# Kernel optimization log

Hardware: AMD Instinct MI355X
Metric: run time of the kernel (lower is better)

The kernel has to match this reference:

```python
import jax, jax.numpy as jnp
import numpy as np

B, S, D, H = 8, 1024, 1024, 16
DH = D // H
LN_EPS = 1e-5
SLOPE = 0.01  # nn.LeakyReLU default negative_slope


def _ln(x, g, b):
    m = x.mean(-1, keepdims=True)
    v = ((x - m) ** 2).mean(-1, keepdims=True)
    return (x - m) / jnp.sqrt(v + LN_EPS) * g + b


def _leaky(x):
    return jnp.where(x >= 0, x, SLOPE * x)


def setup_inputs() -> dict:
    key = jax.random.key(0)
    ks = jax.random.split(key, 6)
    q = jax.random.normal(ks[0], (B, S, D), dtype=jnp.float32)
    masks = jnp.ones((B, S), dtype=jnp.int32)  # all-valid mask (masked_fill is a no-op)
    w1 = jax.random.normal(ks[1], (D, D), dtype=jnp.float32) * 0.02
    b1 = jnp.zeros((D,), jnp.float32)
    w2 = jax.random.normal(ks[2], (D, D), dtype=jnp.float32) * 0.02
    b2 = jnp.zeros((D,), jnp.float32)
    ones = jnp.ones((D,), jnp.float32)
    zeros = jnp.zeros((D,), jnp.float32)
    return dict(q=q, masks=masks,
                w1=w1, b1=b1, ln1_g=ones, ln1_b=zeros,
                w2=w2, b2=b2, ln2_g=ones, ln2_b=zeros,
                anf_g=ones, anf_b=zeros,
                an1_g=ones, an1_b=zeros,
                an2_g=ones, an2_b=zeros)


def reference(q, masks, w1, b1, ln1_g, ln1_b, w2, b2, ln2_g, ln2_b,
              anf_g, anf_b, an1_g, an1_b, an2_g, an2_b):
    # --- multi-head cosine-similarity attention (k = v = q, no projections) ---
    qh = q.reshape(B, S, H, DH).transpose(0, 2, 1, 3)  # (B,H,S,DH) == separate_heads
    qn = qh / jnp.clip(jnp.linalg.norm(qh, axis=-1, keepdims=True), 1e-8)
    # cosine similarity scores, softmax over keys
    w = jax.nn.softmax(jnp.einsum('bhqd,bhkd->bhqk', qn, qn), axis=-1)
    # masked_fill AFTER softmax (faithful to source: mask per (batch, query))
    w = jnp.where(masks[:, None, :, None] == 0, jnp.float32(-1e9), w)
    heads = jnp.einsum('bhqk,bhkd->bhqd', w, qh)
    attn = heads.transpose(0, 2, 1, 3).reshape(B, S, D)  # concat_heads
    # --- add_norm1 (dropout=0.5 but eval mode => identity) ---
    y1 = _ln(q + attn, an1_g, an1_b)
    # --- PositionWiseFFN: Linear->LN->LeakyReLU x2, then internal AddNorm ---
    h = _leaky(_ln(y1 @ w1 + b1, ln1_g, ln1_b))
    y = _leaky(_ln(h @ w2 + b2, ln2_g, ln2_b))
    y2 = _ln(y1 + y, anf_g, anf_b)
    # --- add_norm2 ---
    return _ln(y1 + y2, an2_g, an2_b)
```

## Files before the change

kernel.cpp:

```cpp
#include <hip/hip_runtime.h>
#include <hip/hip_bf16.h>

#define BB 8
#define SS 1024
#define DD 1024
#define HH 16

typedef __attribute__((ext_vector_type(8))) short short8;
typedef __attribute__((ext_vector_type(8))) __bf16 bf16x8;
typedef __attribute__((ext_vector_type(4))) float f32x4;

__device__ inline float bf2f(unsigned short h){
  unsigned u = ((unsigned)h) << 16;
  return __builtin_bit_cast(float, u);
}
__device__ inline unsigned short f2bf(float f){
  unsigned u = __builtin_bit_cast(unsigned, f);
  u += 0x7fffu + ((u >> 16) & 1u);
  return (unsigned short)(u >> 16);
}
__device__ inline f32x4 mfma16(short8 a, short8 b, f32x4 c){
  return __builtin_amdgcn_mfma_f32_16x16x32_bf16(
      __builtin_bit_cast(bf16x8, a), __builtin_bit_cast(bf16x8, b), c, 0, 0, 0);
}

__global__ __launch_bounds__(256) void prep_w(const float* __restrict__ w1,
                                              const float* __restrict__ w2,
                                              unsigned short* __restrict__ w1T,
                                              unsigned short* __restrict__ w2T){
  __shared__ float tile[64][65];
  const float* src = blockIdx.z ? w2 : w1;
  unsigned short* dst = blockIdx.z ? w2T : w1T;
  int k0 = blockIdx.x * 64, n0 = blockIdx.y * 64;
  int tx = threadIdx.x & 63, ty = threadIdx.x >> 6;
#pragma unroll
  for (int r = 0; r < 16; ++r)
    tile[ty + 4*r][tx] = src[(k0 + ty + 4*r) * DD + n0 + tx];
  __syncthreads();
#pragma unroll
  for (int r = 0; r < 16; ++r)
    dst[(n0 + ty + 4*r) * DD + k0 + tx] = f2bf(tile[tx][ty + 4*r]);
}

__global__ __launch_bounds__(256) void prep_q(const float* __restrict__ q,
                                              unsigned short* __restrict__ kf,
                                              unsigned short* __restrict__ vf){
  __shared__ float tile[64][65];
  __shared__ float rinv[64];
  int bh = blockIdx.x >> 4, st = blockIdx.x & 15;
  int b = bh >> 4, h = bh & 15;
  int t = threadIdx.x;
  int tx = t & 63, ty = t >> 6;
  int srow = b * SS + st * 64;
#pragma unroll
  for (int r = 0; r < 16; ++r)
    tile[ty + 4*r][tx] = q[(size_t)(srow + ty + 4*r) * DD + h * 64 + tx];
  __syncthreads();
  {
    int s = t >> 2, p = t & 3;
    float ssum = 0.f;
#pragma unroll
    for (int i = 0; i < 16; ++i){ float v = tile[s][p*16 + i]; ssum += v * v; }
    ssum += __shfl_xor(ssum, 1);
    ssum += __shfl_xor(ssum, 2);
    if (p == 0) rinv[s] = 1.0f / fmaxf(sqrtf(ssum), 1e-8f);
  }
  __syncthreads();
#pragma unroll
  for (int v = 0; v < 2; ++v){
    int idx = t * 2 + v;
    int c_l = idx >> 6, lane = idx & 63;
    int hf = c_l & 1, ch = c_l >> 1;
    int s = ch * 16 + (lane & 15);
    int d0 = hf * 32 + (lane >> 4) * 8;
    float rv = rinv[s];
    short8 o;
#pragma unroll
    for (int e = 0; e < 8; ++e) o[e] = (short)f2bf(tile[s][d0 + e] * rv);
    *(short8*)(kf + ((size_t)(bh * 128 + st * 8 + c_l) * 64 + lane) * 8) = o;
  }
#pragma unroll
  for (int v = 0; v < 2; ++v){
    int idx = t * 2 + v;
    int kt2 = idx >> 8, db = (idx >> 6) & 3, lane = idx & 63;
    int d = db * 16 + (lane & 15);
    int k0 = kt2 * 32 + (lane >> 4) * 8;
    short8 o;
#pragma unroll
    for (int e = 0; e < 8; ++e) o[e] = (short)f2bf(tile[k0 + e][d]);
    *(short8*)(vf + ((size_t)((bh * 32 + st * 2 + kt2) * 4 + db) * 512 + lane * 8)) = o;
  }
}

__global__ __launch_bounds__(512, 8) void attn_kern(const unsigned short* __restrict__ kf,
                                                    const unsigned short* __restrict__ vf,
                                                    const int* __restrict__ masks,
                                                    unsigned short* __restrict__ attnb){
  __shared__ unsigned short Kb[2][4][64 * 8];
  __shared__ unsigned short Vb[2][4][64 * 8];
  __shared__ unsigned short Pw[8][16 * 40];
  __shared__ int anym;
  const int bh = blockIdx.x, b = bh >> 4, h = bh & 15;
  const int sq = blockIdx.y * 128;
  const int t = threadIdx.x, w = t >> 6, l = t & 63;
  const int lr = l & 15, lg = l >> 4;
  if (t == 0) anym = 0;
  __syncthreads();
  if (t < 128 && masks[b * SS + sq + t] == 0) anym = 1;

  short8 aQ[2];
#pragma unroll
  for (int hf = 0; hf < 2; ++hf)
    aQ[hf] = *(const short8*)(kf +
        ((size_t)(bh * 128 + (blockIdx.y * 8 + w) * 2 + hf) * 64 + l) * 8);

  if (w < 4){
    const unsigned short* srcK = kf + ((size_t)(bh * 128 + w) * 64 + l) * 8;
    __builtin_amdgcn_global_load_lds((const __attribute__((address_space(1))) void*)srcK,
        (__attribute__((address_space(3))) void*)(&Kb[0][w][0]), 16, 0, 0);
  } else {
    const unsigned short* srcV = vf + ((size_t)((bh * 32 + 0) * 4 + (w - 4)) * 512 + l * 8);
    __builtin_amdgcn_global_load_lds((const __attribute__((address_space(1))) void*)srcV,
        (__attribute__((address_space(3))) void*)(&Vb[0][w - 4][0]), 16, 0, 0);
  }
  __syncthreads();

  f32x4 o[4] = {};
  f32x4 rsum = {0.f, 0.f, 0.f, 0.f};
  unsigned short* pw = &Pw[w][0];

  for (int it = 0; it < 32; ++it){
    const int cur = it & 1, nxt = cur ^ 1;
    if (it + 1 < 32){
      if (w < 4){
        const unsigned short* srcK = kf + ((size_t)(bh * 128 + (it + 1) * 4 + w) * 64 + l) * 8;
        __builtin_amdgcn_global_load_lds((const __attribute__((address_space(1))) void*)srcK,
            (__attribute__((address_space(3))) void*)(&Kb[nxt][w][0]), 16, 0, 0);
      } else {
        const unsigned short* srcV = vf + ((size_t)((bh * 32 + (it + 1)) * 4 + (w - 4)) * 512 + l * 8);
        __builtin_amdgcn_global_load_lds((const __attribute__((address_space(1))) void*)srcV,
            (__attribute__((address_space(3))) void*)(&Vb[nxt][w - 4][0]), 16, 0, 0);
      }
    }
    short8 bK[2][2];
#pragma unroll
    for (int cc = 0; cc < 2; ++cc)
#pragma unroll
      for (int hf = 0; hf < 2; ++hf)
        bK[cc][hf] = *(const short8*)&Kb[cur][cc * 2 + hf][l * 8];
    f32x4 sc[2];
#pragma unroll
    for (int cc = 0; cc < 2; ++cc){
      f32x4 z = {0.f, 0.f, 0.f, 0.f};
      z = mfma16(aQ[0], bK[cc][0], z);
      z = mfma16(aQ[1], bK[cc][1], z);
      sc[cc] = z;
    }
#pragma unroll
    for (int cc = 0; cc < 2; ++cc)
#pragma unroll
      for (int j = 0; j < 4; ++j){
        float pv = __expf(sc[cc][j] - 1.0f);
        rsum[j] += pv;
        pw[(lg * 4 + j) * 40 + cc * 16 + lr] = f2bf(pv);
      }
    short8 aP = *(const short8*)&pw[lr * 40 + lg * 8];
#pragma unroll
    for (int db = 0; db < 4; ++db){
      short8 bV = *(const short8*)&Vb[cur][db][l * 8];
      o[db] = mfma16(aP, bV, o[db]);
    }
    __syncthreads();
  }

  f32x4 inv;
#pragma unroll
  for (int j = 0; j < 4; ++j){
    float r = rsum[j];
    r += __shfl_xor(r, 1); r += __shfl_xor(r, 2);
    r += __shfl_xor(r, 4); r += __shfl_xor(r, 8);
    inv[j] = 1.0f / r;
  }
#pragma unroll
  for (int db = 0; db < 4; ++db)
#pragma unroll
    for (int j = 0; j < 4; ++j){
      int row = sq + w * 16 + lg * 4 + j;
      float val = o[db][j] * inv[j];
      if (anym && masks[b * SS + row] == 0){
        float vs = 0.f;
        for (int kt = 0; kt < 32; ++kt)
          for (int part = 0; part < 4; ++part){
            const unsigned short* vp = vf +
                ((size_t)((bh * 32 + kt) * 4 + db) * 512 + (part * 16 + lr) * 8);
            for (int e = 0; e < 8; ++e) vs += bf2f(vp[e]);
          }
        val = -1e9f * vs;
      }
      attnb[(size_t)(b * SS + row) * DD + h * 64 + db * 16 + lr] = f2bf(val);
    }
}

__device__ inline float2 block_reduce2(float a, float bq){
  __shared__ float sm[8];
#pragma unroll
  for (int off = 1; off < 64; off <<= 1){
    a += __shfl_xor(a, off);
    bq += __shfl_xor(bq, off);
  }
  int w = threadIdx.x >> 6;
  if ((threadIdx.x & 63) == 0){ sm[2*w] = a; sm[2*w + 1] = bq; }
  __syncthreads();
  float2 r;
  r.x = sm[0] + sm[2] + sm[4] + sm[6];
  r.y = sm[1] + sm[3] + sm[5] + sm[7];
  __syncthreads();
  return r;
}

__global__ __launch_bounds__(256) void addnorm1(const float* __restrict__ q,
                                                const unsigned short* __restrict__ attnb,
                                                const float* __restrict__ g,
                                                const float* __restrict__ bt,
                                                unsigned short* __restrict__ y1b){
  int row = blockIdx.x, t = threadIdx.x;
  float4 qv = *(const float4*)(q + (size_t)row * DD + t * 4);
  ushort4 av = *(const ushort4*)(attnb + (size_t)row * DD + t * 4);
  float x[4] = { qv.x + bf2f(av.x), qv.y + bf2f(av.y), qv.z + bf2f(av.z), qv.w + bf2f(av.w) };
  float s = 0.f, ssq = 0.f;
#pragma unroll
  for (int i = 0; i < 4; ++i){ s += x[i]; ssq += x[i] * x[i]; }
  float2 r = block_reduce2(s, ssq);
  float m = r.x * (1.0f / DD);
  float rs = rsqrtf(r.y * (1.0f / DD) - m * m + 1e-5f);
  float4 gv = *(const float4*)(g + t * 4);
  float4 bv = *(const float4*)(bt + t * 4);
  float y[4] = { (x[0]-m)*rs*gv.x + bv.x, (x[1]-m)*rs*gv.y + bv.y,
                 (x[2]-m)*rs*gv.z + bv.z, (x[3]-m)*rs*gv.w + bv.w };
  ushort4 ob = { f2bf(y[0]), f2bf(y[1]), f2bf(y[2]), f2bf(y[3]) };
  *(ushort4*)(y1b + (size_t)row * DD + t * 4) = ob;
}

__global__ __launch_bounds__(256, 2) void gemm_bias(const unsigned short* __restrict__ X,
                                                    const unsigned short* __restrict__ WT,
                                                    const float* __restrict__ bias,
                                                    unsigned short* __restrict__ out){
  __shared__ unsigned short As[128 * 32];
  __shared__ unsigned short Bs[128 * 32];
  int t = threadIdx.x, l = t & 63, w = t >> 6;
  int wm = w >> 1, wn = w & 1;
  int lr = l & 15, lg = l >> 4;
  int bm = blockIdx.x * 128, bn = blockIdx.y * 128;
  f32x4 acc[4][4] = {};
  int r = t >> 2, cb = (t & 3) * 8;
  for (int kt = 0; kt < 32; ++kt){
    __syncthreads();
    {
      const unsigned short* ga0 = X  + (size_t)(bm +      r) * 1024 + kt * 32 + cb;
      const unsigned short* ga1 = X  + (size_t)(bm + 64 + r) * 1024 + kt * 32 + cb;
      const unsigned short* gb0 = WT + (size_t)(bn +      r) * 1024 + kt * 32 + cb;
      const unsigned short* gb1 = WT + (size_t)(bn + 64 + r) * 1024 + kt * 32 + cb;
      __builtin_amdgcn_global_load_lds((const __attribute__((address_space(1))) void*)ga0,
          (__attribute__((address_space(3))) void*)((char*)As + w * 1024), 16, 0, 0);
      __builtin_amdgcn_global_load_lds((const __attribute__((address_space(1))) void*)ga1,
          (__attribute__((address_space(3))) void*)((char*)As + 4096 + w * 1024), 16, 0, 0);
      __builtin_amdgcn_global_load_lds((const __attribute__((address_space(1))) void*)gb0,
          (__attribute__((address_space(3))) void*)((char*)Bs + w * 1024), 16, 0, 0);
      __builtin_amdgcn_global_load_lds((const __attribute__((address_space(1))) void*)gb1,
          (__attribute__((address_space(3))) void*)((char*)Bs + 4096 + w * 1024), 16, 0, 0);
    }
    __syncthreads();
    short8 aA[4], bB[4];
#pragma unroll
    for (int i = 0; i < 4; ++i)
      aA[i] = *(const short8*)&As[(wm * 64 + i * 16 + lr) * 32 + lg * 8];
#pragma unroll
    for (int i = 0; i < 4; ++i)
      bB[i] = *(const short8*)&Bs[(wn * 64 + i * 16 + lr) * 32 + lg * 8];
#pragma unroll
    for (int mi = 0; mi < 4; ++mi)
#pragma unroll
      for (int ni = 0; ni < 4; ++ni)
        acc[mi][ni] = mfma16(aA[mi], bB[ni], acc[mi][ni]);
  }
#pragma unroll
  for (int ni = 0; ni < 4; ++ni){
    int col = bn + wn * 64 + ni * 16 + lr;
    float bv = bias[col];
#pragma unroll
    for (int mi = 0; mi < 4; ++mi){
      int row0 = bm + wm * 64 + mi * 16 + lg * 4;
#pragma unroll
      for (int j = 0; j < 4; ++j)
        out[(size_t)(row0 + j) * 1024 + col] = f2bf(acc[mi][ni][j] + bv);
    }
  }
}

__global__ __launch_bounds__(256) void ln_leaky(const unsigned short* __restrict__ in,
                                                const float* __restrict__ g,
                                                const float* __restrict__ bt,
                                                unsigned short* __restrict__ out){
  int row = blockIdx.x, t = threadIdx.x;
  ushort4 iv = *(const ushort4*)(in + (size_t)row * DD + t * 4);
  float x[4] = { bf2f(iv.x), bf2f(iv.y), bf2f(iv.z), bf2f(iv.w) };
  float s = 0.f, ssq = 0.f;
#pragma unroll
  for (int i = 0; i < 4; ++i){ s += x[i]; ssq += x[i] * x[i]; }
  float2 r = block_reduce2(s, ssq);
  float m = r.x * (1.0f / DD);
  float rs = rsqrtf(r.y * (1.0f / DD) - m * m + 1e-5f);
  float4 gv = *(const float4*)(g + t * 4);
  float4 bv = *(const float4*)(bt + t * 4);
  ushort4 ov;
  {
    float v0 = (x[0]-m)*rs*gv.x + bv.x; v0 = v0 >= 0.f ? v0 : 0.01f*v0; ov.x = f2bf(v0);
    float v1 = (x[1]-m)*rs*gv.y + bv.y; v1 = v1 >= 0.f ? v1 : 0.01f*v1; ov.y = f2bf(v1);
    float v2 = (x[2]-m)*rs*gv.z + bv.z; v2 = v2 >= 0.f ? v2 : 0.01f*v2; ov.z = f2bf(v2);
    float v3 = (x[3]-m)*rs*gv.w + bv.w; v3 = v3 >= 0.f ? v3 : 0.01f*v3; ov.w = f2bf(v3);
  }
  *(ushort4*)(out + (size_t)row * DD + t * 4) = ov;
}

__global__ __launch_bounds__(256) void final_kern(const unsigned short* __restrict__ g2,
                                                  const unsigned short* __restrict__ y1,
                                                  const float* __restrict__ ln2g, const float* __restrict__ ln2b,
                                                  const float* __restrict__ anfg, const float* __restrict__ anfb,
                                                  const float* __restrict__ an2g, const float* __restrict__ an2b,
                                                  float* __restrict__ out){
  int row = blockIdx.x, t = threadIdx.x;
  ushort4 iv = *(const ushort4*)(g2 + (size_t)row * DD + t * 4);
  ushort4 y1v = *(const ushort4*)(y1 + (size_t)row * DD + t * 4);
  float x[4] = { bf2f(iv.x), bf2f(iv.y), bf2f(iv.z), bf2f(iv.w) };
  float yy1[4] = { bf2f(y1v.x), bf2f(y1v.y), bf2f(y1v.z), bf2f(y1v.w) };
  float s = 0.f, ssq = 0.f;
#pragma unroll
  for (int i = 0; i < 4; ++i){ s += x[i]; ssq += x[i]*x[i]; }
  float2 r = block_reduce2(s, ssq);
  float m = r.x * (1.0f / DD);
  float rs = rsqrtf(r.y * (1.0f / DD) - m*m + 1e-5f);
  float4 gv = *(const float4*)(ln2g + t * 4);
  float4 bv = *(const float4*)(ln2b + t * 4);
  float y[4] = { (x[0]-m)*rs*gv.x + bv.x, (x[1]-m)*rs*gv.y + bv.y,
                 (x[2]-m)*rs*gv.z + bv.z, (x[3]-m)*rs*gv.w + bv.w };
#pragma unroll
  for (int i = 0; i < 4; ++i) y[i] = y[i] >= 0.f ? y[i] : 0.01f*y[i];

  float tv[4]; s = 0.f; ssq = 0.f;
#pragma unroll
  for (int i = 0; i < 4; ++i){ tv[i] = yy1[i] + y[i]; s += tv[i]; ssq += tv[i]*tv[i]; }
  r = block_reduce2(s, ssq);
  m = r.x * (1.0f / DD);
  rs = rsqrtf(r.y * (1.0f / DD) - m*m + 1e-5f);
  gv = *(const float4*)(anfg + t * 4);
  bv = *(const float4*)(anfb + t * 4);
  float y2[4] = { (tv[0]-m)*rs*gv.x + bv.x, (tv[1]-m)*rs*gv.y + bv.y,
                  (tv[2]-m)*rs*gv.z + bv.z, (tv[3]-m)*rs*gv.w + bv.w };

  float u[4]; s = 0.f; ssq = 0.f;
#pragma unroll
  for (int i = 0; i < 4; ++i){ u[i] = yy1[i] + y2[i]; s += u[i]; ssq += u[i]*u[i]; }
  r = block_reduce2(s, ssq);
  m = r.x * (1.0f / DD);
  rs = rsqrtf(r.y * (1.0f / DD) - m*m + 1e-5f);
  gv = *(const float4*)(an2g + t * 4);
  bv = *(const float4*)(an2b + t * 4);
  float4 ov = { (u[0]-m)*rs*gv.x + bv.x, (u[1]-m)*rs*gv.y + bv.y,
                (u[2]-m)*rs*gv.z + bv.z, (u[3]-m)*rs*gv.w + bv.w };
  *(float4*)(out + (size_t)row * DD + t * 4) = ov;
}

extern "C" void kernel_launch(void* const* d_in, const int* in_sizes, int n_in,
                              void* d_out, int out_size, void* d_ws, size_t ws_size,
                              hipStream_t stream){
  const float* q    = (const float*)d_in[0];
  const int* masks  = (const int*)d_in[1];
  const float* w1   = (const float*)d_in[2];
  const float* b1   = (const float*)d_in[3];
  const float* ln1g = (const float*)d_in[4];
  const float* ln1b = (const float*)d_in[5];
  const float* w2   = (const float*)d_in[6];
  const float* b2   = (const float*)d_in[7];
  const float* ln2g = (const float*)d_in[8];
  const float* ln2b = (const float*)d_in[9];
  const float* anfg = (const float*)d_in[10];
  const float* anfb = (const float*)d_in[11];
  const float* an1g = (const float*)d_in[12];
  const float* an1b = (const float*)d_in[13];
  const float* an2g = (const float*)d_in[14];
  const float* an2b = (const float*)d_in[15];

  char* ws = (char*)d_ws;
  unsigned short* w1T  = (unsigned short*)(ws + 0);
  unsigned short* w2T  = (unsigned short*)(ws + 2097152);
  unsigned short* kf   = (unsigned short*)(ws + 4194304);
  unsigned short* vf   = (unsigned short*)(ws + 20971520);
  unsigned short* attn = (unsigned short*)(ws + 37748736);
  unsigned short* y1b  = (unsigned short*)(ws + 54525952);
  unsigned short* g1   = kf;
  unsigned short* hbuf = vf;
  unsigned short* g2   = attn;
  float* outp = (float*)d_out;

  prep_w<<<dim3(16, 16, 2), 256, 0, stream>>>(w1, w2, w1T, w2T);
  prep_q<<<dim3(2048), 256, 0, stream>>>(q, kf, vf);
  attn_kern<<<dim3(128, 8), 512, 0, stream>>>(kf, vf, masks, attn);
  addnorm1<<<dim3(8192), 256, 0, stream>>>(q, attn, an1g, an1b, y1b);
  gemm_bias<<<dim3(64, 8), 256, 0, stream>>>(y1b, w1T, b1, g1);
  ln_leaky<<<dim3(8192), 256, 0, stream>>>(g1, ln1g, ln1b, hbuf);
  gemm_bias<<<dim3(64, 8), 256, 0, stream>>>(hbuf, w2T, b2, g2);
  final_kern<<<dim3(8192), 256, 0, stream>>>(g2, y1b, ln2g, ln2b, anfg, anfb, an2g, an2b, outp);
}
```

Baseline: 167.0 us.

## Compute transposed scores so softmax probabilities stay in registers for PV MFMA

The attention kernel now computes S^T by swapping MFMA operands (K as A, Q as B), with the Q rows permuted in prep_q. The exponentiated scores then already sit in the register layout the PV MFMA needs as its A operand. This removes the per-wave LDS round-trip for P and the per-row shuffle reductions, at the cost of a cross-lane shuffle to redistribute the row inverses. Separately, prep_q writes a bf16 copy of q that addnorm1 reads instead of fp32, halving that read but adding an extra write and bf16 rounding of the residual.

```diff
diff --git a/kernel.cpp b/kernel.cpp
--- a/kernel.cpp
+++ b/kernel.cpp
@@ -22,6 +22,10 @@
 __device__ inline f32x4 mfma16(short8 a, short8 b, f32x4 c){
   return __builtin_amdgcn_mfma_f32_16x16x32_bf16(
       __builtin_bit_cast(bf16x8, a), __builtin_bit_cast(bf16x8, b), c, 0, 0, 0);
+}
+__device__ inline void gld_lds16(const unsigned short* g, unsigned short* l){
+  __builtin_amdgcn_global_load_lds((const __attribute__((address_space(1))) void*)g,
+      (__attribute__((address_space(3))) void*)l, 16, 0, 0);
 }
 
 __global__ __launch_bounds__(256) void prep_w(const float* __restrict__ w1,
@@ -44,7 +48,8 @@
 
 __global__ __launch_bounds__(256) void prep_q(const float* __restrict__ q,
                                               unsigned short* __restrict__ kf,
-                                              unsigned short* __restrict__ vf){
+                                              unsigned short* __restrict__ vf,
+                                              unsigned short* __restrict__ qb){
   __shared__ float tile[64][65];
   __shared__ float rinv[64];
   int bh = blockIdx.x >> 4, st = blockIdx.x & 15;
@@ -67,12 +72,16 @@
   }
   __syncthreads();
 #pragma unroll
+  for (int r = 0; r < 16; ++r)
+    qb[(size_t)(srow + ty + 4*r) * DD + h * 64 + tx] = f2bf(tile[ty + 4*r][tx]);
+#pragma unroll
   for (int v = 0; v < 2; ++v){
     int idx = t * 2 + v;
     int c_l = idx >> 6, lane = idx & 63;
-    int hf = c_l & 1, ch = c_l >> 1;
-    int s = ch * 16 + (lane & 15);
-    int d0 = hf * 32 + (lane >> 4) * 8;
+    int g2 = c_l >> 2, c = (c_l >> 1) & 1, hf = c_l & 1;
+    int lrq = lane & 15, lgq = lane >> 4;
+    int s = g2 * 32 + (lrq >> 2) * 8 + c * 4 + (lrq & 3);
+    int d0 = hf * 32 + lgq * 8;
     float rv = rinv[s];
     short8 o;
 #pragma unroll
@@ -92,112 +101,98 @@
   }
 }
 
-__global__ __launch_bounds__(512, 8) void attn_kern(const unsigned short* __restrict__ kf,
+__global__ __launch_bounds__(512, 6) void attn_kern(const unsigned short* __restrict__ kf,
                                                     const unsigned short* __restrict__ vf,
                                                     const int* __restrict__ masks,
                                                     unsigned short* __restrict__ attnb){
   __shared__ unsigned short Kb[2][4][64 * 8];
   __shared__ unsigned short Vb[2][4][64 * 8];
-  __shared__ unsigned short Pw[8][16 * 40];
   __shared__ int anym;
   const int bh = blockIdx.x, b = bh >> 4, h = bh & 15;
-  const int sq = blockIdx.y * 128;
+  const int by = blockIdx.y;
   const int t = threadIdx.x, w = t >> 6, l = t & 63;
   const int lr = l & 15, lg = l >> 4;
   if (t == 0) anym = 0;
   __syncthreads();
-  if (t < 128 && masks[b * SS + sq + t] == 0) anym = 1;
+  if (t < 128 && masks[b * SS + by * 128 + t] == 0) anym = 1;
 
   short8 aQ[2];
 #pragma unroll
   for (int hf = 0; hf < 2; ++hf)
     aQ[hf] = *(const short8*)(kf +
-        ((size_t)(bh * 128 + (blockIdx.y * 8 + w) * 2 + hf) * 64 + l) * 8);
+        ((size_t)(bh * 128 + by * 16 + (w >> 1) * 4 + (w & 1) * 2 + hf) * 64 + l) * 8);
 
   if (w < 4){
-    const unsigned short* srcK = kf + ((size_t)(bh * 128 + w) * 64 + l) * 8;
-    __builtin_amdgcn_global_load_lds((const __attribute__((address_space(1))) void*)srcK,
-        (__attribute__((address_space(3))) void*)(&Kb[0][w][0]), 16, 0, 0);
+    gld_lds16(kf + ((size_t)(bh * 128 + w) * 64 + l) * 8, &Kb[0][w][0]);
   } else {
-    const unsigned short* srcV = vf + ((size_t)((bh * 32 + 0) * 4 + (w - 4)) * 512 + l * 8);
-    __builtin_amdgcn_global_load_lds((const __attribute__((address_space(1))) void*)srcV,
-        (__attribute__((address_space(3))) void*)(&Vb[0][w - 4][0]), 16, 0, 0);
+    gld_lds16(vf + ((size_t)((bh * 32 + 0) * 4 + (w - 4)) * 512 + l * 8), &Vb[0][w - 4][0]);
   }
   __syncthreads();
 
   f32x4 o[4] = {};
-  f32x4 rsum = {0.f, 0.f, 0.f, 0.f};
-  unsigned short* pw = &Pw[w][0];
+  float rs0 = 0.f, rs1 = 0.f;
 
   for (int it = 0; it < 32; ++it){
     const int cur = it & 1, nxt = cur ^ 1;
     if (it + 1 < 32){
-      if (w < 4){
-        const unsigned short* srcK = kf + ((size_t)(bh * 128 + (it + 1) * 4 + w) * 64 + l) * 8;
-        __builtin_amdgcn_global_load_lds((const __attribute__((address_space(1))) void*)srcK,
-            (__attribute__((address_space(3))) void*)(&Kb[nxt][w][0]), 16, 0, 0);
-      } else {
-        const unsigned short* srcV = vf + ((size_t)((bh * 32 + (it + 1)) * 4 + (w - 4)) * 512 + l * 8);
-        __builtin_amdgcn_global_load_lds((const __attribute__((address_space(1))) void*)srcV,
-            (__attribute__((address_space(3))) void*)(&Vb[nxt][w - 4][0]), 16, 0, 0);
+      if (w < 4)
+        gld_lds16(kf + ((size_t)(bh * 128 + (it + 1) * 4 + w) * 64 + l) * 8, &Kb[nxt][w][0]);
+      else
+        gld_lds16(vf + ((size_t)((bh * 32 + it + 1) * 4 + (w - 4)) * 512 + l * 8), &Vb[nxt][w - 4][0]);
+    }
+    f32x4 sc[2];
+#pragma unroll
+    for (int c = 0; c < 2; ++c){
+      short8 a0 = *(const short8*)&Kb[cur][c * 2 + 0][l * 8];
+      short8 a1 = *(const short8*)&Kb[cur][c * 2 + 1][l * 8];
+      f32x4 z = {0.f, 0.f, 0.f, 0.f};
+      z = mfma16(a0, aQ[0], z);
+      z = mfma16(a1, aQ[1], z);
+      sc[c] = z;
+    }
+    bf16x8 pav;
+#pragma unroll
+    for (int c = 0; c < 2; ++c)
+#pragma unroll
+      for (int j = 0; j < 4; ++j){
+        float pv = __expf(sc[c][j] - 1.0f);
+        if (j & 1) rs1 += pv; else rs0 += pv;
+        pav[c * 4 + j] = (__bf16)pv;
       }
-    }
-    short8 bK[2][2];
-#pragma unroll
-    for (int cc = 0; cc < 2; ++cc)
-#pragma unroll
-      for (int hf = 0; hf < 2; ++hf)
-        bK[cc][hf] = *(const short8*)&Kb[cur][cc * 2 + hf][l * 8];
-    f32x4 sc[2];
-#pragma unroll
-    for (int cc = 0; cc < 2; ++cc){
-      f32x4 z = {0.f, 0.f, 0.f, 0.f};
-      z = mfma16(aQ[0], bK[cc][0], z);
-      z = mfma16(aQ[1], bK[cc][1], z);
-      sc[cc] = z;
-    }
-#pragma unroll
-    for (int cc = 0; cc < 2; ++cc)
-#pragma unroll
-      for (int j = 0; j < 4; ++j){
-        float pv = __expf(sc[cc][j] - 1.0f);
-        rsum[j] += pv;
-        pw[(lg * 4 + j) * 40 + cc * 16 + lr] = f2bf(pv);
-      }
-    short8 aP = *(const short8*)&pw[lr * 40 + lg * 8];
+    short8 pa = __builtin_bit_cast(short8, pav);
 #pragma unroll
     for (int db = 0; db < 4; ++db){
       short8 bV = *(const short8*)&Vb[cur][db][l * 8];
-      o[db] = mfma16(aP, bV, o[db]);
+      o[db] = mfma16(pa, bV, o[db]);
     }
     __syncthreads();
   }
 
-  f32x4 inv;
-#pragma unroll
-  for (int j = 0; j < 4; ++j){
-    float r = rsum[j];
-    r += __shfl_xor(r, 1); r += __shfl_xor(r, 2);
-    r += __shfl_xor(r, 4); r += __shfl_xor(r, 8);
-    inv[j] = 1.0f / r;
-  }
+  float rsum = rs0 + rs1;
+  rsum += __shfl_xor(rsum, 16);
+  rsum += __shfl_xor(rsum, 32);
+  float inv = 1.0f / rsum;
+  float invj[4];
+#pragma unroll
+  for (int j = 0; j < 4; ++j) invj[j] = __shfl(inv, lg * 4 + j);
+
 #pragma unroll
   for (int db = 0; db < 4; ++db)
 #pragma unroll
     for (int j = 0; j < 4; ++j){
-      int row = sq + w * 16 + lg * 4 + j;
-      float val = o[db][j] * inv[j];
-      if (anym && masks[b * SS + row] == 0){
+      int qrow = by * 128 + (w >> 1) * 32 + lg * 8 + (w & 1) * 4 + j;
+      float val = o[db][j] * invj[j];
+      if (anym && masks[b * SS + qrow] == 0){
         float vs = 0.f;
         for (int kt = 0; kt < 32; ++kt)
-          for (int part = 0; part < 4; ++part){
+          for (int lgp = 0; lgp < 4; ++lgp){
             const unsigned short* vp = vf +
-                ((size_t)((bh * 32 + kt) * 4 + db) * 512 + (part * 16 + lr) * 8);
+                ((size_t)((bh * 32 + kt) * 4 + db) * 512 + (lgp * 16 + lr) * 8);
             for (int e = 0; e < 8; ++e) vs += bf2f(vp[e]);
           }
         val = -1e9f * vs;
       }
-      attnb[(size_t)(b * SS + row) * DD + h * 64 + db * 16 + lr] = f2bf(val);
+      attnb[(size_t)(b * SS + qrow) * DD + h * 64 + db * 16 + lr] = f2bf(val);
     }
 }
 
@@ -218,15 +213,16 @@
   return r;
 }
 
-__global__ __launch_bounds__(256) void addnorm1(const float* __restrict__ q,
+__global__ __launch_bounds__(256) void addnorm1(const unsigned short* __restrict__ qb,
                                                 const unsigned short* __restrict__ attnb,
                                                 const float* __restrict__ g,
                                                 const float* __restrict__ bt,
                                                 unsigned short* __restrict__ y1b){
   int row = blockIdx.x, t = threadIdx.x;
-  float4 qv = *(const float4*)(q + (size_t)row * DD + t * 4);
+  ushort4 qv = *(const ushort4*)(qb + (size_t)row * DD + t * 4);
   ushort4 av = *(const ushort4*)(attnb + (size_t)row * DD + t * 4);
-  float x[4] = { qv.x + bf2f(av.x), qv.y + bf2f(av.y), qv.z + bf2f(av.z), qv.w + bf2f(av.w) };
+  float x[4] = { bf2f(qv.x) + bf2f(av.x), bf2f(qv.y) + bf2f(av.y),
+                 bf2f(qv.z) + bf2f(av.z), bf2f(qv.w) + bf2f(av.w) };
   float s = 0.f, ssq = 0.f;
 #pragma unroll
   for (int i = 0; i < 4; ++i){ s += x[i]; ssq += x[i] * x[i]; }
@@ -397,15 +393,16 @@
   unsigned short* vf   = (unsigned short*)(ws + 20971520);
   unsigned short* attn = (unsigned short*)(ws + 37748736);
   unsigned short* y1b  = (unsigned short*)(ws + 54525952);
+  unsigned short* qb   = (unsigned short*)(ws + 71303168);
   unsigned short* g1   = kf;
   unsigned short* hbuf = vf;
   unsigned short* g2   = attn;
   float* outp = (float*)d_out;
 
   prep_w<<<dim3(16, 16, 2), 256, 0, stream>>>(w1, w2, w1T, w2T);
-  prep_q<<<dim3(2048), 256, 0, stream>>>(q, kf, vf);
+  prep_q<<<dim3(2048), 256, 0, stream>>>(q, kf, vf, qb);
   attn_kern<<<dim3(128, 8), 512, 0, stream>>>(kf, vf, masks, attn);
-  addnorm1<<<dim3(8192), 256, 0, stream>>>(q, attn, an1g, an1b, y1b);
+  addnorm1<<<dim3(8192), 256, 0, stream>>>(qb, attn, an1g, an1b, y1b);
   gemm_bias<<<dim3(64, 8), 256, 0, stream>>>(y1b, w1T, b1, g1);
   ln_leaky<<<dim3(8192), 256, 0, stream>>>(g1, ln1g, ln1b, hbuf);
   gemm_bias<<<dim3(64, 8), 256, 0, stream>>>(hbuf, w2T, b2, g2);
```

Result: faster. 162.9 us (-2.5%).
